# Kernel optimization log

Measured on AMD Instinct MI355X. Metric: run time of the kernel, lower is better.

Reference implementation:

```python
import jax, jax.numpy as jnp
import numpy as np


def setup_inputs() -> dict:
    key = jax.random.key(0)
    k1, k2, k3, k4 = jax.random.split(key, 4)
    n, b, h, f = 8, 64, 128, 256
    hs = 64
    x = jax.random.normal(k1, (n, b, h, f), dtype=jnp.float32)
    # torch Linear weights are (out, in); store transposed as (in, out) for x @ W
    Wq = jax.random.normal(k2, (f, hs), dtype=jnp.float32) * (6.0 / (f + hs)) ** 0.5
    Wk = jax.random.normal(k3, (f, hs), dtype=jnp.float32) * (6.0 / (f + hs)) ** 0.5
    Wv = jax.random.normal(k4, (f, hs), dtype=jnp.float32) * (6.0 / (f + hs)) ** 0.5
    return {"x": x, "Wq": Wq, "Wk": Wk, "Wv": Wv}


def reference(x, Wq, Wk, Wv):
    # x: (n, b, h, f). NOTE: scale uses f = n_embd (as in the source), not head_size.
    f = x.shape[-1]
    scale = f ** (-0.5)
    Q = jnp.einsum('nbhf,fd->nbhd', x, Wq)  # (n, b, h, hs)
    K = jnp.einsum('nbhf,fd->nbhd', x, Wk)
    V = jnp.einsum('nbhf,fd->nbhd', x, Wv)
    # alphas[i, j, b, p, q] = sum_d Q[j,b,p,d] * K[i,b,q,d] * scale
    scores = jnp.einsum('jbpd,ibqd->ijbpq', Q, K) * scale  # (n, n, b, h, h)
    alphas = jax.nn.softmax(scores, axis=-1)
    # out[i, j, b, p, d] = sum_q alphas[i,j,b,p,q] V[i,b,q,d]; then sum over i
    o = jnp.einsum('ijbpq,ibqd->jbpd', alphas, V)  # (n, b, h, hs)
    return o
```

## Files before the change

### kernel.cpp

```cpp
#include <hip/hip_runtime.h>
#include <cstdint>

#define N_SEQ 8
#define B_DIM 64
#define H_DIM 128
#define F_DIM 256
#define HS 64

typedef __attribute__((ext_vector_type(8))) short short8;
typedef __attribute__((ext_vector_type(4))) float floatx4;

__device__ __forceinline__ ushort f2bf(float f) {
    union { float f; uint32_t u; } v; v.f = f;
    uint32_t r = v.u + 0x7FFF + ((v.u >> 16) & 1);
    return (ushort)(r >> 16);
}

__global__ __launch_bounds__(256) void prep_w(
    const float* __restrict__ Wq, const float* __restrict__ Wk,
    const float* __restrict__ Wv, ushort* __restrict__ Wtb)
{
    const int n = blockIdx.x;
    const float* W = (n < 64) ? Wq : (n < 128) ? Wk : Wv;
    const int c = n & 63;
    const int k = threadIdx.x;
    Wtb[n * 256 + k] = f2bf(W[k * 64 + c]);
}

#define XS_STRIDE 264
__global__ __launch_bounds__(256, 4) void proj_mfma(
    const float* __restrict__ x, const ushort* __restrict__ Wtb,
    ushort* __restrict__ Qb, ushort* __restrict__ Kb, ushort* __restrict__ Vtb)
{
    __shared__ ushort xs[64 * XS_STRIDE];
    const int t = threadIdx.x;
    const int blk = blockIdx.x;
    const int64_t row0 = (int64_t)blk * 64;

    const float4* xg = (const float4*)(x + row0 * F_DIM);
    #pragma unroll
    for (int u = 0; u < 8; ++u) {
        const int idx = t + 256 * u;
        const int row = idx >> 5;
        const int c8 = (idx & 31) * 8;
        const float4 a = xg[idx * 2];
        const float4 b = xg[idx * 2 + 1];
        *(ushort4*)&xs[row * XS_STRIDE + c8] =
            make_ushort4(f2bf(a.x), f2bf(a.y), f2bf(a.z), f2bf(a.w));
        *(ushort4*)&xs[row * XS_STRIDE + c8 + 4] =
            make_ushort4(f2bf(b.x), f2bf(b.y), f2bf(b.z), f2bf(b.w));
    }
    __syncthreads();

    const int w = t >> 6, lane = t & 63;
    const int q16 = lane >> 4, l16 = lane & 15;
    const int n0 = w * 48;

    floatx4 acc[4][3];
    #pragma unroll
    for (int mt = 0; mt < 4; ++mt)
        #pragma unroll
        for (int nt = 0; nt < 3; ++nt) acc[mt][nt] = (floatx4){0.f, 0.f, 0.f, 0.f};

    short8 nb[3];
    #pragma unroll
    for (int nt = 0; nt < 3; ++nt)
        nb[nt] = *(const short8*)&Wtb[(n0 + nt * 16 + l16) * 256 + q16 * 8];

    for (int ks = 0; ks < 8; ++ks) {
        short8 cur[3];
        #pragma unroll
        for (int nt = 0; nt < 3; ++nt) cur[nt] = nb[nt];
        if (ks < 7) {
            #pragma unroll
            for (int nt = 0; nt < 3; ++nt)
                nb[nt] = *(const short8*)&Wtb[(n0 + nt * 16 + l16) * 256 + (ks + 1) * 32 + q16 * 8];
        }
        #pragma unroll
        for (int mt = 0; mt < 4; ++mt) {
            const short8 afr = *(const short8*)&xs[(mt * 16 + l16) * XS_STRIDE + ks * 32 + q16 * 8];
            #pragma unroll
            for (int nt = 0; nt < 3; ++nt)
                acc[mt][nt] = __builtin_amdgcn_mfma_f32_16x16x32_bf16(afr, cur[nt], acc[mt][nt], 0, 0, 0);
        }
    }

    const float qscale = 0.0625f * 1.44269504f;
    #pragma unroll
    for (int mt = 0; mt < 4; ++mt) {
        const int64_t g = row0 + mt * 16 + q16 * 4;
        #pragma unroll
        for (int nt = 0; nt < 3; ++nt) {
            const int ntb = n0 + nt * 16;
            const int n = ntb + l16;
            if (ntb < 64) {
                #pragma unroll
                for (int r = 0; r < 4; ++r)
                    Qb[(g + r) * 64 + n] = f2bf(acc[mt][nt][r] * qscale);
            } else if (ntb < 128) {
                #pragma unroll
                for (int r = 0; r < 4; ++r)
                    Kb[(g + r) * 64 + (n - 64)] = f2bf(acc[mt][nt][r]);
            } else {
                const int d = n - 128;
                const int ib = (int)(g >> 7);
                const int h = (int)(g & 127);
                *(ushort4*)&Vtb[((int64_t)(ib * 64 + d)) * 128 + h] =
                    make_ushort4(f2bf(acc[mt][nt][0]), f2bf(acc[mt][nt][1]),
                                 f2bf(acc[mt][nt][2]), f2bf(acc[mt][nt][3]));
            }
        }
    }
}

#define KS_STRIDE 68
#define VT_STRIDE 132
#define PS_STRIDE 36
__global__ __launch_bounds__(256, 4) void attn_mfma(
    const ushort* __restrict__ Qb, const ushort* __restrict__ Kb,
    const ushort* __restrict__ Vtb, float* __restrict__ out)
{
    __shared__ ushort Ks[128 * KS_STRIDE];
    __shared__ ushort Vt[64 * VT_STRIDE];
    __shared__ ushort Ps[4][16 * PS_STRIDE];

    const int t = threadIdx.x;
    const int blk = blockIdx.x;
    const int jb = blk >> 1;
    const int hh = blk & 1;
    const int b = jb & 63;
    const int w = t >> 6, lane = t & 63;
    const int q16 = lane >> 4, l16 = lane & 15;
    ushort* Psw = &Ps[w][0];

    const int qrow0 = jb * H_DIM + hh * 64 + w * 16;
    short8 qa[2];
    #pragma unroll
    for (int ks = 0; ks < 2; ++ks)
        qa[ks] = *(const short8*)&Qb[(qrow0 + l16) * 64 + ks * 32 + q16 * 8];

    floatx4 of[4];
    #pragma unroll
    for (int nt = 0; nt < 4; ++nt) of[nt] = (floatx4){0.f, 0.f, 0.f, 0.f};

    for (int i = 0; i < N_SEQ; ++i) {
        const int ib = i * B_DIM + b;
        __syncthreads();
        {
            const uint4* ksrc = (const uint4*)(Kb + (int64_t)ib * H_DIM * HS);
            const uint4* vsrc = (const uint4*)(Vtb + (int64_t)ib * HS * H_DIM);
            #pragma unroll
            for (int u = 0; u < 4; ++u) {
                const int idx = t + 256 * u;
                const int krow = idx >> 3, kc = (idx & 7) * 8;
                *(uint4*)&Ks[krow * KS_STRIDE + kc] = ksrc[idx];
                const int vrow = idx >> 4, vc = (idx & 15) * 8;
                *(uint4*)&Vt[vrow * VT_STRIDE + vc] = vsrc[idx];
            }
        }
        __syncthreads();

        floatx4 sf[8];
        #pragma unroll
        for (int nt = 0; nt < 8; ++nt) sf[nt] = (floatx4){0.f, 0.f, 0.f, 0.f};
        #pragma unroll
        for (int ks = 0; ks < 2; ++ks)
            #pragma unroll
            for (int nt = 0; nt < 8; ++nt) {
                const short8 bk = *(const short8*)&Ks[(nt * 16 + l16) * KS_STRIDE + ks * 32 + q16 * 8];
                sf[nt] = __builtin_amdgcn_mfma_f32_16x16x32_bf16(qa[ks], bk, sf[nt], 0, 0, 0);
            }

        #pragma unroll
        for (int nt = 0; nt < 8; ++nt)
            #pragma unroll
            for (int r = 0; r < 4; ++r) sf[nt][r] = __builtin_amdgcn_exp2f(sf[nt][r]);

        float inv[4];
        #pragma unroll
        for (int r = 0; r < 4; ++r) {
            float l = 0.f;
            #pragma unroll
            for (int nt = 0; nt < 8; ++nt) l += sf[nt][r];
            #pragma unroll
            for (int msk = 1; msk < 16; msk <<= 1) l += __shfl_xor(l, msk);
            inv[r] = __builtin_amdgcn_rcpf(l);
        }

        #pragma unroll
        for (int kq = 0; kq < 4; ++kq) {
            #pragma unroll
            for (int nt2 = 0; nt2 < 2; ++nt2) {
                const int nt = kq * 2 + nt2;
                #pragma unroll
                for (int r = 0; r < 4; ++r)
                    Psw[(q16 * 4 + r) * PS_STRIDE + nt2 * 16 + l16] = f2bf(sf[nt][r] * inv[r]);
            }
            const short8 ap = *(const short8*)&Psw[l16 * PS_STRIDE + q16 * 8];
            #pragma unroll
            for (int nt = 0; nt < 4; ++nt) {
                const short8 bv = *(const short8*)&Vt[(nt * 16 + l16) * VT_STRIDE + kq * 32 + q16 * 8];
                of[nt] = __builtin_amdgcn_mfma_f32_16x16x32_bf16(ap, bv, of[nt], 0, 0, 0);
            }
        }
    }

    #pragma unroll
    for (int nt = 0; nt < 4; ++nt)
        #pragma unroll
        for (int r = 0; r < 4; ++r)
            out[((int64_t)qrow0 + q16 * 4 + r) * HS + nt * 16 + l16] = of[nt][r];
}

extern "C" void kernel_launch(void* const* d_in, const int* in_sizes, int n_in,
                              void* d_out, int out_size, void* d_ws, size_t ws_size,
                              hipStream_t stream)
{
    const float* x  = (const float*)d_in[0];
    const float* Wq = (const float*)d_in[1];
    const float* Wk = (const float*)d_in[2];
    const float* Wv = (const float*)d_in[3];
    float* out = (float*)d_out;

    const size_t qkv = (size_t)N_SEQ * B_DIM * H_DIM * HS;
    ushort* Qb  = (ushort*)d_ws;
    ushort* Kb  = Qb + qkv;
    ushort* Vtb = Kb + qkv;
    ushort* Wtb = Vtb + qkv;

    prep_w<<<192, 256, 0, stream>>>(Wq, Wk, Wv, Wtb);
    proj_mfma<<<(N_SEQ * B_DIM * H_DIM) / 64, 256, 0, stream>>>(x, Wtb, Qb, Kb, Vtb);
    attn_mfma<<<N_SEQ * B_DIM * 2, 256, 0, stream>>>(Qb, Kb, Vtb, out);
}
```

Measured before the change: 168.1 us.

## Prefetch next K/V tile into registers, transpose score MFMA, remap blocks per XCD

Attention blocks are remapped so that each XCD handles a contiguous group of batch indices, which should improve L2 reuse of the K/V tiles those blocks share. The next iteration's K/V tile is loaded into registers while the current tile is being computed, hiding global load latency behind the MFMA work. The score MFMAs now compute S transposed, so each lane holds one query column. This lets the softmax row sum run with two shuffles instead of four per row, lets P be written as packed ushort4 stores, and lets the output be stored as float4. The cost is extra register pressure from the prefetch buffers.

```diff
diff --git a/kernel.cpp b/kernel.cpp
--- a/kernel.cpp
+++ b/kernel.cpp
@@ -115,20 +115,24 @@
 
 #define KS_STRIDE 68
 #define VT_STRIDE 132
-#define PS_STRIDE 36
+#define PT_STRIDE 40
 __global__ __launch_bounds__(256, 4) void attn_mfma(
     const ushort* __restrict__ Qb, const ushort* __restrict__ Kb,
     const ushort* __restrict__ Vtb, float* __restrict__ out)
 {
     __shared__ ushort Ks[128 * KS_STRIDE];
     __shared__ ushort Vt[64 * VT_STRIDE];
-    __shared__ ushort Ps[4][16 * PS_STRIDE];
+    __shared__ ushort Ps[4][16 * PT_STRIDE];
 
     const int t = threadIdx.x;
     const int blk = blockIdx.x;
-    const int jb = blk >> 1;
-    const int hh = blk & 1;
-    const int b = jb & 63;
+    const int xcd = blk & 7;
+    const int hh  = (blk >> 3) & 1;
+    const int bhi = (blk >> 4) & 7;
+    const int j   = blk >> 7;
+    const int b   = xcd * 8 + bhi;
+    const int jb  = j * 64 + b;
+
     const int w = t >> 6, lane = t & 63;
     const int q16 = lane >> 4, l16 = lane & 15;
     ushort* Psw = &Ps[w][0];
@@ -141,25 +145,33 @@
 
     floatx4 of[4];
     #pragma unroll
-    for (int nt = 0; nt < 4; ++nt) of[nt] = (floatx4){0.f, 0.f, 0.f, 0.f};
+    for (int mt = 0; mt < 4; ++mt) of[mt] = (floatx4){0.f, 0.f, 0.f, 0.f};
+
+    uint4 pk[4], pv[4];
+    {
+        const uint4* ks = (const uint4*)(Kb + (int64_t)b * H_DIM * HS);
+        const uint4* vs = (const uint4*)(Vtb + (int64_t)b * HS * H_DIM);
+        #pragma unroll
+        for (int u = 0; u < 4; ++u) { pk[u] = ks[t + 256 * u]; pv[u] = vs[t + 256 * u]; }
+    }
 
     for (int i = 0; i < N_SEQ; ++i) {
-        const int ib = i * B_DIM + b;
         __syncthreads();
-        {
-            const uint4* ksrc = (const uint4*)(Kb + (int64_t)ib * H_DIM * HS);
-            const uint4* vsrc = (const uint4*)(Vtb + (int64_t)ib * HS * H_DIM);
-            #pragma unroll
-            for (int u = 0; u < 4; ++u) {
-                const int idx = t + 256 * u;
-                const int krow = idx >> 3, kc = (idx & 7) * 8;
-                *(uint4*)&Ks[krow * KS_STRIDE + kc] = ksrc[idx];
-                const int vrow = idx >> 4, vc = (idx & 15) * 8;
-                *(uint4*)&Vt[vrow * VT_STRIDE + vc] = vsrc[idx];
-            }
+        #pragma unroll
+        for (int u = 0; u < 4; ++u) {
+            const int idx = t + 256 * u;
+            *(uint4*)&Ks[(idx >> 3) * KS_STRIDE + (idx & 7) * 8] = pk[u];
+            *(uint4*)&Vt[(idx >> 4) * VT_STRIDE + (idx & 15) * 8] = pv[u];
         }
         __syncthreads();
 
+        if (i < N_SEQ - 1) {
+            const uint4* ks = (const uint4*)(Kb + ((int64_t)(i + 1) * B_DIM + b) * H_DIM * HS);
+            const uint4* vs = (const uint4*)(Vtb + ((int64_t)(i + 1) * B_DIM + b) * HS * H_DIM);
+            #pragma unroll
+            for (int u = 0; u < 4; ++u) { pk[u] = ks[t + 256 * u]; pv[u] = vs[t + 256 * u]; }
+        }
+
         floatx4 sf[8];
         #pragma unroll
         for (int nt = 0; nt < 8; ++nt) sf[nt] = (floatx4){0.f, 0.f, 0.f, 0.f};
@@ -167,8 +179,8 @@
         for (int ks = 0; ks < 2; ++ks)
             #pragma unroll
             for (int nt = 0; nt < 8; ++nt) {
-                const short8 bk = *(const short8*)&Ks[(nt * 16 + l16) * KS_STRIDE + ks * 32 + q16 * 8];
-                sf[nt] = __builtin_amdgcn_mfma_f32_16x16x32_bf16(qa[ks], bk, sf[nt], 0, 0, 0);
+                const short8 ak = *(const short8*)&Ks[(nt * 16 + l16) * KS_STRIDE + ks * 32 + q16 * 8];
+                sf[nt] = __builtin_amdgcn_mfma_f32_16x16x32_bf16(ak, qa[ks], sf[nt], 0, 0, 0);
             }
 
         #pragma unroll
@@ -176,40 +188,37 @@
             #pragma unroll
             for (int r = 0; r < 4; ++r) sf[nt][r] = __builtin_amdgcn_exp2f(sf[nt][r]);
 
-        float inv[4];
-        #pragma unroll
-        for (int r = 0; r < 4; ++r) {
-            float l = 0.f;
-            #pragma unroll
-            for (int nt = 0; nt < 8; ++nt) l += sf[nt][r];
-            #pragma unroll
-            for (int msk = 1; msk < 16; msk <<= 1) l += __shfl_xor(l, msk);
-            inv[r] = __builtin_amdgcn_rcpf(l);
-        }
+        float l = 0.f;
+        #pragma unroll
+        for (int nt = 0; nt < 8; ++nt)
+            #pragma unroll
+            for (int r = 0; r < 4; ++r) l += sf[nt][r];
+        l += __shfl_xor(l, 16);
+        l += __shfl_xor(l, 32);
+        const float inv = __builtin_amdgcn_rcpf(l);
 
         #pragma unroll
         for (int kq = 0; kq < 4; ++kq) {
             #pragma unroll
-            for (int nt2 = 0; nt2 < 2; ++nt2) {
-                const int nt = kq * 2 + nt2;
-                #pragma unroll
-                for (int r = 0; r < 4; ++r)
-                    Psw[(q16 * 4 + r) * PS_STRIDE + nt2 * 16 + l16] = f2bf(sf[nt][r] * inv[r]);
-            }
-            const short8 ap = *(const short8*)&Psw[l16 * PS_STRIDE + q16 * 8];
-            #pragma unroll
-            for (int nt = 0; nt < 4; ++nt) {
-                const short8 bv = *(const short8*)&Vt[(nt * 16 + l16) * VT_STRIDE + kq * 32 + q16 * 8];
-                of[nt] = __builtin_amdgcn_mfma_f32_16x16x32_bf16(ap, bv, of[nt], 0, 0, 0);
-            }
-        }
-    }
-
-    #pragma unroll
-    for (int nt = 0; nt < 4; ++nt)
-        #pragma unroll
-        for (int r = 0; r < 4; ++r)
-            out[((int64_t)qrow0 + q16 * 4 + r) * HS + nt * 16 + l16] = of[nt][r];
+            for (int tt = 0; tt < 2; ++tt) {
+                const int nt = kq * 2 + tt;
+                *(ushort4*)&Psw[l16 * PT_STRIDE + tt * 16 + q16 * 4] =
+                    make_ushort4(f2bf(sf[nt][0] * inv), f2bf(sf[nt][1] * inv),
+                                 f2bf(sf[nt][2] * inv), f2bf(sf[nt][3] * inv));
+            }
+            const short8 bp = *(const short8*)&Psw[l16 * PT_STRIDE + q16 * 8];
+            #pragma unroll
+            for (int mt = 0; mt < 4; ++mt) {
+                const short8 av = *(const short8*)&Vt[(mt * 16 + l16) * VT_STRIDE + kq * 32 + q16 * 8];
+                of[mt] = __builtin_amdgcn_mfma_f32_16x16x32_bf16(av, bp, of[mt], 0, 0, 0);
+            }
+        }
+    }
+
+    #pragma unroll
+    for (int mt = 0; mt < 4; ++mt)
+        *(float4*)&out[((int64_t)qrow0 + l16) * HS + mt * 16 + q16 * 4] =
+            make_float4(of[mt][0], of[mt][1], of[mt][2], of[mt][3]);
 }
 
 extern "C" void kernel_launch(void* const* d_in, const int* in_sizes, int n_in,
```

After: 205.4 us. +22.2%, slower.
